# Kernel tuning notes

Measured on AMD Instinct MI355X. Metric: run time of the kernel, lower is better.

## Reference

```python
import jax, jax.numpy as jnp
import numpy as np

B, S, D = 4, 2048, 1024
H = 16
DK = D // H  # 64

def setup_inputs() -> dict:
    key = jax.random.key(0)
    ks = jax.random.split(key, 5)
    scale = 0.02
    return {
        "x": jax.random.normal(ks[0], (B, S, D), dtype=jnp.float32),
        "Wq": jax.random.normal(ks[1], (D, D), dtype=jnp.float32) * scale,
        "Wk": jax.random.normal(ks[2], (D, D), dtype=jnp.float32) * scale,
        "Wv": jax.random.normal(ks[3], (D, D), dtype=jnp.float32) * scale,
        "Wo": jax.random.normal(ks[4], (D, D), dtype=jnp.float32) * scale,
    }

def reference(x, Wq, Wk, Wv, Wo):
    b, s, d = x.shape
    h, dk = H, DK
    # torch nn.Linear(bias=False): y = x @ W.T
    q = (x @ Wq.T).reshape(b, s, h, dk).transpose(0, 2, 1, 3)  # [b,h,s,dk]
    k = (x @ Wk.T).reshape(b, s, h, dk).transpose(0, 2, 1, 3)
    v = (x @ Wv.T).reshape(b, s, h, dk).transpose(0, 2, 1, 3)
    scores = jnp.einsum('bhqd,bhkd->bhqk', q, k) * (dk ** -0.5)
    causal = jnp.triu(jnp.ones((s, s), dtype=bool), k=1)  # True = masked out
    scores = jnp.where(causal, -jnp.inf, scores)
    probs = jax.nn.softmax(scores, axis=-1)
    attn = jnp.einsum('bhqk,bhkd->bhqd', probs, v)  # [b,h,s,dk]
    attn = attn.transpose(0, 2, 1, 3).reshape(b, s, d)
    return attn @ Wo.T
```

## Files before the change

kernel.cpp:

```cpp
#include <hip/hip_runtime.h>

typedef __attribute__((ext_vector_type(8))) short bf16x8;
typedef __attribute__((ext_vector_type(4))) float f32x4;
typedef __attribute__((ext_vector_type(2))) unsigned int u32x2;
typedef unsigned int u32;
typedef unsigned short u16;

constexpr int Bb = 4, S = 2048, D = 1024, H = 16, DK = 64, M = Bb * S;

#if __has_builtin(__builtin_amdgcn_exp2f)
#define EXP2F __builtin_amdgcn_exp2f
#else
#define EXP2F exp2f
#endif

__device__ __forceinline__ u16 f2bf(float f) {
  u32 u = __float_as_uint(f);
  return (u16)((u + 0x7fffu + ((u >> 16) & 1u)) >> 16);
}

__device__ __forceinline__ u32 cvt_pk_bf16(float a, float b) {
  u32 r;
  asm("v_cvt_pk_bf16_f32 %0, %1, %2" : "=v"(r) : "v"(a), "v"(b));
  return r;
}

__device__ __forceinline__ void gld_lds16(const u16* g, u16* l) {
  __builtin_amdgcn_global_load_lds((const __attribute__((address_space(1))) u32*)g,
                                   (__attribute__((address_space(3))) u32*)l, 16, 0, 0);
}

__global__ void cast_kernel(const float* __restrict__ s, u16* __restrict__ d, int n) {
  int i = (blockIdx.x * blockDim.x + threadIdx.x) * 4;
  if (i >= n) return;
  float4 f = *(const float4*)(s + i);
  ushort4 o;
  o.x = f2bf(f.x); o.y = f2bf(f.y); o.z = f2bf(f.z); o.w = f2bf(f.w);
  *(ushort4*)(d + i) = o;
}

struct CastArgs { const float* s[4]; u16* d[4]; float sc[4]; };
__global__ void cast4_kernel(CastArgs a) {
  int i = (blockIdx.x * blockDim.x + threadIdx.x) * 4;
  int w = i >> 20;
  int off = i & ((1 << 20) - 1);
  float sc = a.sc[w];
  float4 f = *(const float4*)(a.s[w] + off);
  ushort4 o;
  o.x = f2bf(f.x * sc); o.y = f2bf(f.y * sc); o.z = f2bf(f.z * sc); o.w = f2bf(f.w * sc);
  *(ushort4*)(a.d[w] + off) = o;
}

template <bool OUTF32>
__device__ __forceinline__ void gemm_core(const u16* __restrict__ A,
                                          const u16* __restrict__ Bt,
                                          float* __restrict__ Cf, u16* __restrict__ Cb,
                                          int Nn, int Kk, int m0, int n0,
                                          u16* As, u16* Bs) {
  const int tid = threadIdx.x, wave = tid >> 6, lane = tid & 63;
  const int quad = lane >> 4, col = lane & 15;
  const int wm = wave >> 1, wn = wave & 1;

  f32x4 acc[4][4];
#pragma unroll
  for (int i = 0; i < 4; i++)
#pragma unroll
    for (int j = 0; j < 4; j++) acc[i][j] = (f32x4){0.f, 0.f, 0.f, 0.f};

  for (int k0 = 0; k0 < Kk; k0 += 64) {
#pragma unroll
    for (int j = 0; j < 4; j++) {
      int g = (wave * 4 + j) * 64;
      int gl = g + lane;
      int r = gl >> 3, sl = gl & 7;
      int kof = (sl ^ (r & 7)) * 8;
      const u16* ga = A + (size_t)(m0 + r) * Kk + k0 + kof;
      gld_lds16(ga, &As[g * 8]);
      const u16* gb = Bt + (size_t)(n0 + r) * Kk + k0 + kof;
      gld_lds16(gb, &Bs[g * 8]);
    }
    __syncthreads();
#pragma unroll
    for (int kb = 0; kb < 2; kb++) {
      bf16x8 af[4], bfr[4];
#pragma unroll
      for (int mi = 0; mi < 4; mi++) {
        int R = wm * 64 + mi * 16 + col;
        af[mi] = *(const bf16x8*)&As[R * 64 + (((kb * 4 + quad) ^ (R & 7)) << 3)];
      }
#pragma unroll
      for (int ni = 0; ni < 4; ni++) {
        int R = wn * 64 + ni * 16 + col;
        bfr[ni] = *(const bf16x8*)&Bs[R * 64 + (((kb * 4 + quad) ^ (R & 7)) << 3)];
      }
#pragma unroll
      for (int mi = 0; mi < 4; mi++)
#pragma unroll
        for (int ni = 0; ni < 4; ni++)
          acc[mi][ni] = __builtin_amdgcn_mfma_f32_16x16x32_bf16(af[mi], bfr[ni], acc[mi][ni], 0, 0, 0);
    }
    __syncthreads();
  }
#pragma unroll
  for (int mi = 0; mi < 4; mi++)
#pragma unroll
    for (int ni = 0; ni < 4; ni++)
#pragma unroll
      for (int r = 0; r < 4; r++) {
        int row = m0 + wm * 64 + mi * 16 + quad * 4 + r;
        int cc = n0 + wn * 64 + ni * 16 + col;
        float v = acc[mi][ni][r];
        if (OUTF32) Cf[(size_t)row * Nn + cc] = v;
        else Cb[(size_t)row * Nn + cc] = f2bf(v);
      }
}

struct QkvArgs { const u16* bt[3]; u16* c[3]; };
__global__ __launch_bounds__(256) void gemm_qkv(const u16* __restrict__ A, QkvArgs q) {
  __shared__ __align__(16) u16 As[128 * 64];
  __shared__ __align__(16) u16 Bs[128 * 64];
  int sel = blockIdx.x >> 3;
  int n0 = (blockIdx.x & 7) * 128, m0 = blockIdx.y * 128;
  gemm_core<false>(A, q.bt[sel], nullptr, q.c[sel], D, D, m0, n0, As, Bs);
}

__global__ __launch_bounds__(256) void gemm_f32(const u16* __restrict__ A,
                                                const u16* __restrict__ Bt,
                                                float* __restrict__ C) {
  __shared__ __align__(16) u16 As[128 * 64];
  __shared__ __align__(16) u16 Bs[128 * 64];
  gemm_core<true>(A, Bt, C, nullptr, D, D, blockIdx.y * 128, blockIdx.x * 128, As, Bs);
}

__global__ __launch_bounds__(256) void attn_kernel(const u16* __restrict__ Q,
                                                   const u16* __restrict__ K,
                                                   const u16* __restrict__ V,
                                                   u16* __restrict__ O) {
  __shared__ __align__(16) u16 Ks[2][2][64 * 32];
  __shared__ __align__(16) u16 Vt[2][64 * 64];
  __shared__ __align__(16) u16 Pw[4][32 * 64];
  const int tid = threadIdx.x, wave = tid >> 6, lane = tid & 63;
  const int quad = lane >> 4, col = lane & 15;
  const int bh = blockIdx.x, b = bh >> 4, h = bh & 15;
  const int pair = blockIdx.y;
  const size_t base = (size_t)b * S * D + h * DK;

  const int vk0 = (tid & 31) * 2;
  const int vdg = tid >> 5;

  bf16x8 bones;
#pragma unroll
  for (int e = 0; e < 8; e++) bones[e] = (short)0x3F80;

  const int rsw = col & 7;
  const int ksl = ((quad ^ ((col >> 1) & 3)) & 3) << 3;
  const u16* kbase[2] = { &Ks[0][0][col * 32 + ksl], &Ks[1][0][col * 32 + ksl] };
  const int vsl0 = ((quad ^ rsw) & 7) << 3;
  const int vsl1 = (((4 + quad) ^ rsw) & 7) << 3;
  const u16* vbase[2] = { &Vt[0][col * 64], &Vt[1][col * 64] };
  u16* pww[2] = { &Pw[wave][col * 64 + (quad & 1) * 4],
                  &Pw[wave][(16 + col) * 64 + (quad & 1) * 4] };
  int swof[4];
#pragma unroll
  for (int n16 = 0; n16 < 4; n16++)
    swof[n16] = (((n16 * 2 + (quad >> 1)) ^ rsw) & 7) << 3;
  const u16* apbase[2] = { &Pw[wave][col * 64], &Pw[wave][(16 + col) * 64] };
  const int kk = tid >> 2;
  const int dch = (tid & 3) ^ ((kk >> 1) & 3);
  const int cb = wave * 64;
  u16* dk[2][2] = { { &Ks[0][0][cb * 8], &Ks[0][1][cb * 8] },
                    { &Ks[1][0][cb * 8], &Ks[1][1][cb * 8] } };
  const int kgrp = vk0 >> 3, kin = vk0 & 7;
  u16* vwb[2] = { &Vt[0][vdg * 8 * 64 + kin], &Vt[1][vdg * 8 * 64 + kin] };
  int vwof[8];
#pragma unroll
  for (int e = 0; e < 8; e++) vwof[e] = e * 64 + ((kgrp ^ e) & 7) * 8;

  auto vstage = [&](const int buf, bf16x8 r0, bf16x8 r1) {
    u16* wb = vwb[buf];
#pragma unroll
    for (int e = 0; e < 8; e++) {
      u32 val = ((u32)(u16)r0[e]) | ((u32)(u16)r1[e] << 16);
      *(u32*)(wb + vwof[e]) = val;
    }
  };

  for (int half = 0; half < 2; half++) {
    const int qb = half ? pair : 15 - pair;
    const int qw = qb * 128 + wave * 32;
    const int nkt = 2 * qb + 2;

    bf16x8 aq[2][2];
#pragma unroll
    for (int mi = 0; mi < 2; mi++)
#pragma unroll
      for (int kb = 0; kb < 2; kb++)
        aq[mi][kb] = *(const bf16x8*)(Q + base + (size_t)(qw + mi * 16 + col) * D + kb * 32 + quad * 8);

    f32x4 ao[2][4], lacc[2];
#pragma unroll
    for (int mi = 0; mi < 2; mi++) {
      lacc[mi] = (f32x4){0.f, 0.f, 0.f, 0.f};
#pragma unroll
      for (int dg = 0; dg < 4; dg++) ao[mi][dg] = (f32x4){0.f, 0.f, 0.f, 0.f};
    }

    auto compute = [&](const int BF, int kt) {
      const u16* kbK = kbase[BF];
      bf16x8 bk0[4], bk1[4];
#pragma unroll
      for (int n16 = 0; n16 < 4; n16++) {
        bk0[n16] = *(const bf16x8*)(kbK + n16 * 512);
        bk1[n16] = *(const bf16x8*)(kbK + n16 * 512 + 2048);
      }
      f32x4 sacc[2][4];
#pragma unroll
      for (int qi = 0; qi < 2; qi++)
#pragma unroll
        for (int n16 = 0; n16 < 4; n16++) sacc[qi][n16] = (f32x4){0.f, 0.f, 0.f, 0.f};
      __builtin_amdgcn_s_setprio(1);
#pragma unroll
      for (int qi = 0; qi < 2; qi++)
#pragma unroll
        for (int n16 = 0; n16 < 4; n16++) {
          sacc[qi][n16] = __builtin_amdgcn_mfma_f32_16x16x32_bf16(bk0[n16], aq[qi][0], sacc[qi][n16], 0, 0, 0);
          sacc[qi][n16] = __builtin_amdgcn_mfma_f32_16x16x32_bf16(bk1[n16], aq[qi][1], sacc[qi][n16], 0, 0, 0);
        }
      __builtin_amdgcn_s_setprio(0);
      const bool full = (kt * 64 + 63) <= qw;
#pragma unroll
      for (int qi = 0; qi < 2; qi++) {
        const int qg = qw + qi * 16 + col;
#pragma unroll
        for (int n16 = 0; n16 < 4; n16++) {
          float p0 = EXP2F(sacc[qi][n16][0]);
          float p1 = EXP2F(sacc[qi][n16][1]);
          float p2 = EXP2F(sacc[qi][n16][2]);
          float p3 = EXP2F(sacc[qi][n16][3]);
          if (!full) {
            int kg = kt * 64 + n16 * 16 + quad * 4;
            p0 = (kg + 0 > qg) ? 0.f : p0;
            p1 = (kg + 1 > qg) ? 0.f : p1;
            p2 = (kg + 2 > qg) ? 0.f : p2;
            p3 = (kg + 3 > qg) ? 0.f : p3;
          }
          u32 lo = cvt_pk_bf16(p0, p1);
          u32 hi = cvt_pk_bf16(p2, p3);
          *(u32x2*)(pww[qi] + swof[n16]) = (u32x2){lo, hi};
        }
      }
      const u16* vtB = vbase[BF];
      bf16x8 bv0[4], bv1[4];
#pragma unroll
      for (int dg = 0; dg < 4; dg++) {
        bv0[dg] = *(const bf16x8*)(vtB + dg * 1024 + vsl0);
        bv1[dg] = *(const bf16x8*)(vtB + dg * 1024 + vsl1);
      }
#pragma unroll
      for (int mi = 0; mi < 2; mi++) {
        bf16x8 ap0 = *(const bf16x8*)(apbase[mi] + vsl0);
        bf16x8 ap1 = *(const bf16x8*)(apbase[mi] + vsl1);
        __builtin_amdgcn_s_setprio(1);
#pragma unroll
        for (int dg = 0; dg < 4; dg++) {
          ao[mi][dg] = __builtin_amdgcn_mfma_f32_16x16x32_bf16(ap0, bv0[dg], ao[mi][dg], 0, 0, 0);
          ao[mi][dg] = __builtin_amdgcn_mfma_f32_16x16x32_bf16(ap1, bv1[dg], ao[mi][dg], 0, 0, 0);
        }
        lacc[mi] = __builtin_amdgcn_mfma_f32_16x16x32_bf16(ap0, bones, lacc[mi], 0, 0, 0);
        lacc[mi] = __builtin_amdgcn_mfma_f32_16x16x32_bf16(ap1, bones, lacc[mi], 0, 0, 0);
        __builtin_amdgcn_s_setprio(0);
      }
    };

    bf16x8 vA0, vA1, vB0, vB1;
    const u16* gv = V + base + (size_t)vk0 * D + vdg * 8;
    vA0 = *(const bf16x8*)gv;
    vA1 = *(const bf16x8*)(gv + D);
    __syncthreads();
    const u16* gk = K + base + (size_t)kk * D + dch * 8;
    gld_lds16(gk, dk[0][0]);
    gld_lds16(gk + 32, dk[0][1]);
    gk += (size_t)64 * D;
    vstage(0, vA0, vA1);
    vB0 = *(const bf16x8*)(gv + (size_t)64 * D);
    vB1 = *(const bf16x8*)(gv + (size_t)64 * D + D);
    gv += (size_t)128 * D;

    for (int kt = 0; kt < nkt; kt += 2) {
      __syncthreads();
      {
        gld_lds16(gk, dk[1][0]);
        gld_lds16(gk + 32, dk[1][1]);
        gk += (size_t)64 * D;
        vstage(1, vB0, vB1);
        if (kt + 2 < nkt) {
          vA0 = *(const bf16x8*)gv;
          vA1 = *(const bf16x8*)(gv + D);
          gv += (size_t)64 * D;
        }
        if (kt * 64 <= qw + 31) compute(0, kt);
      }
      __syncthreads();
      {
        const int kt1 = kt + 1;
        if (kt1 + 1 < nkt) {
          gld_lds16(gk, dk[0][0]);
          gld_lds16(gk + 32, dk[0][1]);
          gk += (size_t)64 * D;
          vstage(0, vA0, vA1);
          if (kt1 + 2 < nkt) {
            vB0 = *(const bf16x8*)gv;
            vB1 = *(const bf16x8*)(gv + D);
            gv += (size_t)64 * D;
          }
        }
        if (kt1 * 64 <= qw + 31) compute(1, kt1);
      }
    }
#pragma unroll
    for (int mi = 0; mi < 2; mi++)
#pragma unroll
      for (int r = 0; r < 4; r++) {
        float inv = 1.f / lacc[mi][r];
        int q = qw + mi * 16 + quad * 4 + r;
#pragma unroll
        for (int dg = 0; dg < 4; dg++)
          O[base + (size_t)q * D + dg * 16 + col] = f2bf(ao[mi][dg][r] * inv);
      }
  }
}

extern "C" void kernel_launch(void* const* d_in, const int* in_sizes, int n_in,
                              void* d_out, int out_size, void* d_ws, size_t ws_size,
                              hipStream_t stream) {
  const float* x  = (const float*)d_in[0];
  const float* Wq = (const float*)d_in[1];
  const float* Wk = (const float*)d_in[2];
  const float* Wv = (const float*)d_in[3];
  const float* Wo = (const float*)d_in[4];

  u16* xb  = (u16*)d_ws;
  u16* wqb = xb + (size_t)M * D;
  u16* wkb = wqb + (size_t)D * D;
  u16* wvb = wkb + (size_t)D * D;
  u16* wob = wvb + (size_t)D * D;
  u16* Qb  = wob + (size_t)D * D;
  u16* Kb  = Qb + (size_t)M * D;
  u16* Vb  = Kb + (size_t)M * D;
  u16* Ab  = xb;

  cast_kernel<<<M * D / 1024, 256, 0, stream>>>(x, xb, M * D);
  CastArgs ca;
  ca.s[0] = Wq; ca.s[1] = Wk; ca.s[2] = Wv; ca.s[3] = Wo;
  ca.d[0] = wqb; ca.d[1] = wkb; ca.d[2] = wvb; ca.d[3] = wob;
  ca.sc[0] = 0.18033688011112042f;
  ca.sc[1] = 1.f; ca.sc[2] = 1.f; ca.sc[3] = 1.f;
  cast4_kernel<<<4 * D * D / 1024, 256, 0, stream>>>(ca);

  QkvArgs qa;
  qa.bt[0] = wqb; qa.bt[1] = wkb; qa.bt[2] = wvb;
  qa.c[0] = Qb; qa.c[1] = Kb; qa.c[2] = Vb;
  gemm_qkv<<<dim3(24, M / 128), 256, 0, stream>>>(xb, qa);

  attn_kernel<<<dim3(Bb * H, 8), 256, 0, stream>>>(Qb, Kb, Vb, Ab);

  gemm_f32<<<dim3(D / 128, M / 128), 256, 0, stream>>>(Ab, wob, (float*)d_out);
}
```

Baseline: 247.4 us.

## Stage 128-key blocks per barrier in attention and merge cast kernels

```diff
diff --git a/kernel.cpp b/kernel.cpp
--- a/kernel.cpp
+++ b/kernel.cpp
@@ -30,20 +30,12 @@
                                    (__attribute__((address_space(3))) u32*)l, 16, 0, 0);
 }
 
-__global__ void cast_kernel(const float* __restrict__ s, u16* __restrict__ d, int n) {
-  int i = (blockIdx.x * blockDim.x + threadIdx.x) * 4;
-  if (i >= n) return;
-  float4 f = *(const float4*)(s + i);
-  ushort4 o;
-  o.x = f2bf(f.x); o.y = f2bf(f.y); o.z = f2bf(f.z); o.w = f2bf(f.w);
-  *(ushort4*)(d + i) = o;
-}
-
-struct CastArgs { const float* s[4]; u16* d[4]; float sc[4]; };
-__global__ void cast4_kernel(CastArgs a) {
-  int i = (blockIdx.x * blockDim.x + threadIdx.x) * 4;
-  int w = i >> 20;
-  int off = i & ((1 << 20) - 1);
+struct CastAll { const float* s[5]; u16* d[5]; float sc[5]; };
+__global__ __launch_bounds__(256) void cast_all_kernel(CastAll a) {
+  int bid = blockIdx.x;
+  int w, off;
+  if (bid < 4096) { w = bid >> 10; off = ((bid & 1023) * 256 + threadIdx.x) * 4; }
+  else            { w = 4;         off = ((bid - 4096) * 256 + threadIdx.x) * 4; }
   float sc = a.sc[w];
   float4 f = *(const float4*)(a.s[w] + off);
   ushort4 o;
@@ -136,8 +128,8 @@
                                                    const u16* __restrict__ K,
                                                    const u16* __restrict__ V,
                                                    u16* __restrict__ O) {
-  __shared__ __align__(16) u16 Ks[2][2][64 * 32];
-  __shared__ __align__(16) u16 Vt[2][64 * 64];
+  __shared__ __align__(16) u16 Ks[2][2][2][64 * 32];
+  __shared__ __align__(16) u16 Vt[2][2][64 * 64];
   __shared__ __align__(16) u16 Pw[4][32 * 64];
   const int tid = threadIdx.x, wave = tid >> 6, lane = tid & 63;
   const int quad = lane >> 4, col = lane & 15;
@@ -154,10 +146,22 @@
 
   const int rsw = col & 7;
   const int ksl = ((quad ^ ((col >> 1) & 3)) & 3) << 3;
-  const u16* kbase[2] = { &Ks[0][0][col * 32 + ksl], &Ks[1][0][col * 32 + ksl] };
+  const u16* kbase[2][2];
+  const u16* vbase[2][2];
+  u16* dk[2][2][2];
+  u16* vwb[2][2];
+#pragma unroll
+  for (int bu = 0; bu < 2; bu++)
+#pragma unroll
+    for (int kh = 0; kh < 2; kh++) {
+      kbase[bu][kh] = &Ks[bu][kh][0][col * 32 + ksl];
+      vbase[bu][kh] = &Vt[bu][kh][col * 64];
+      dk[bu][kh][0] = &Ks[bu][kh][0][wave * 64 * 8];
+      dk[bu][kh][1] = &Ks[bu][kh][1][wave * 64 * 8];
+      vwb[bu][kh] = &Vt[bu][kh][vdg * 8 * 64 + (vk0 & 7)];
+    }
   const int vsl0 = ((quad ^ rsw) & 7) << 3;
   const int vsl1 = (((4 + quad) ^ rsw) & 7) << 3;
-  const u16* vbase[2] = { &Vt[0][col * 64], &Vt[1][col * 64] };
   u16* pww[2] = { &Pw[wave][col * 64 + (quad & 1) * 4],
                   &Pw[wave][(16 + col) * 64 + (quad & 1) * 4] };
   int swof[4];
@@ -167,17 +171,12 @@
   const u16* apbase[2] = { &Pw[wave][col * 64], &Pw[wave][(16 + col) * 64] };
   const int kk = tid >> 2;
   const int dch = (tid & 3) ^ ((kk >> 1) & 3);
-  const int cb = wave * 64;
-  u16* dk[2][2] = { { &Ks[0][0][cb * 8], &Ks[0][1][cb * 8] },
-                    { &Ks[1][0][cb * 8], &Ks[1][1][cb * 8] } };
-  const int kgrp = vk0 >> 3, kin = vk0 & 7;
-  u16* vwb[2] = { &Vt[0][vdg * 8 * 64 + kin], &Vt[1][vdg * 8 * 64 + kin] };
+  const int kgrp = vk0 >> 3;
   int vwof[8];
 #pragma unroll
   for (int e = 0; e < 8; e++) vwof[e] = e * 64 + ((kgrp ^ e) & 7) * 8;
 
-  auto vstage = [&](const int buf, bf16x8 r0, bf16x8 r1) {
-    u16* wb = vwb[buf];
+  auto vstage = [&](u16* wb, bf16x8 r0, bf16x8 r1) {
 #pragma unroll
     for (int e = 0; e < 8; e++) {
       u32 val = ((u32)(u16)r0[e]) | ((u32)(u16)r1[e] << 16);
@@ -188,7 +187,7 @@
   for (int half = 0; half < 2; half++) {
     const int qb = half ? pair : 15 - pair;
     const int qw = qb * 128 + wave * 32;
-    const int nkt = 2 * qb + 2;
+    const int n128 = qb + 1;
 
     bf16x8 aq[2][2];
 #pragma unroll
@@ -205,8 +204,8 @@
       for (int dg = 0; dg < 4; dg++) ao[mi][dg] = (f32x4){0.f, 0.f, 0.f, 0.f};
     }
 
-    auto compute = [&](const int BF, int kt) {
-      const u16* kbK = kbase[BF];
+    auto compute = [&](const int BF, const int HH, int kt) {
+      const u16* kbK = kbase[BF][HH];
       bf16x8 bk0[4], bk1[4];
 #pragma unroll
       for (int n16 = 0; n16 < 4; n16++) {
@@ -249,7 +248,7 @@
           *(u32x2*)(pww[qi] + swof[n16]) = (u32x2){lo, hi};
         }
       }
-      const u16* vtB = vbase[BF];
+      const u16* vtB = vbase[BF][HH];
       bf16x8 bv0[4], bv1[4];
 #pragma unroll
       for (int dg = 0; dg < 4; dg++) {
@@ -272,50 +271,69 @@
       }
     };
 
-    bf16x8 vA0, vA1, vB0, vB1;
+    bf16x8 vA0, vA1, vA2, vA3, vB0, vB1, vB2, vB3;
     const u16* gv = V + base + (size_t)vk0 * D + vdg * 8;
     vA0 = *(const bf16x8*)gv;
     vA1 = *(const bf16x8*)(gv + D);
+    vA2 = *(const bf16x8*)(gv + (size_t)64 * D);
+    vA3 = *(const bf16x8*)(gv + (size_t)65 * D);
     __syncthreads();
     const u16* gk = K + base + (size_t)kk * D + dch * 8;
-    gld_lds16(gk, dk[0][0]);
-    gld_lds16(gk + 32, dk[0][1]);
-    gk += (size_t)64 * D;
-    vstage(0, vA0, vA1);
-    vB0 = *(const bf16x8*)(gv + (size_t)64 * D);
-    vB1 = *(const bf16x8*)(gv + (size_t)64 * D + D);
-    gv += (size_t)128 * D;
-
-    for (int kt = 0; kt < nkt; kt += 2) {
+    gld_lds16(gk, dk[0][0][0]);
+    gld_lds16(gk + 32, dk[0][0][1]);
+    gld_lds16(gk + (size_t)64 * D, dk[0][1][0]);
+    gld_lds16(gk + (size_t)64 * D + 32, dk[0][1][1]);
+    gk += (size_t)128 * D;
+    vstage(vwb[0][0], vA0, vA1);
+    vstage(vwb[0][1], vA2, vA3);
+    if (n128 > 1) {
+      vB0 = *(const bf16x8*)(gv + (size_t)128 * D);
+      vB1 = *(const bf16x8*)(gv + (size_t)129 * D);
+      vB2 = *(const bf16x8*)(gv + (size_t)192 * D);
+      vB3 = *(const bf16x8*)(gv + (size_t)193 * D);
+    }
+    gv += (size_t)256 * D;
+
+    for (int t2 = 0; t2 < n128; t2 += 2) {
       __syncthreads();
-      {
-        gld_lds16(gk, dk[1][0]);
-        gld_lds16(gk + 32, dk[1][1]);
-        gk += (size_t)64 * D;
-        vstage(1, vB0, vB1);
-        if (kt + 2 < nkt) {
+      if (t2 + 1 < n128) {
+        gld_lds16(gk, dk[1][0][0]);
+        gld_lds16(gk + 32, dk[1][0][1]);
+        gld_lds16(gk + (size_t)64 * D, dk[1][1][0]);
+        gld_lds16(gk + (size_t)64 * D + 32, dk[1][1][1]);
+        gk += (size_t)128 * D;
+        vstage(vwb[1][0], vB0, vB1);
+        vstage(vwb[1][1], vB2, vB3);
+        if (t2 + 2 < n128) {
           vA0 = *(const bf16x8*)gv;
           vA1 = *(const bf16x8*)(gv + D);
-          gv += (size_t)64 * D;
-        }
-        if (kt * 64 <= qw + 31) compute(0, kt);
-      }
+          vA2 = *(const bf16x8*)(gv + (size_t)64 * D);
+          vA3 = *(const bf16x8*)(gv + (size_t)65 * D);
+          gv += (size_t)128 * D;
+        }
+      }
+      compute(0, 0, 2 * t2);
+      if ((2 * t2 + 1) * 64 <= qw + 31) compute(0, 1, 2 * t2 + 1);
+      if (t2 + 1 >= n128) break;
       __syncthreads();
-      {
-        const int kt1 = kt + 1;
-        if (kt1 + 1 < nkt) {
-          gld_lds16(gk, dk[0][0]);
-          gld_lds16(gk + 32, dk[0][1]);
-          gk += (size_t)64 * D;
-          vstage(0, vA0, vA1);
-          if (kt1 + 2 < nkt) {
-            vB0 = *(const bf16x8*)gv;
-            vB1 = *(const bf16x8*)(gv + D);
-            gv += (size_t)64 * D;
-          }
-        }
-        if (kt1 * 64 <= qw + 31) compute(1, kt1);
-      }
+      if (t2 + 2 < n128) {
+        gld_lds16(gk, dk[0][0][0]);
+        gld_lds16(gk + 32, dk[0][0][1]);
+        gld_lds16(gk + (size_t)64 * D, dk[0][1][0]);
+        gld_lds16(gk + (size_t)64 * D + 32, dk[0][1][1]);
+        gk += (size_t)128 * D;
+        vstage(vwb[0][0], vA0, vA1);
+        vstage(vwb[0][1], vA2, vA3);
+        if (t2 + 3 < n128) {
+          vB0 = *(const bf16x8*)gv;
+          vB1 = *(const bf16x8*)(gv + D);
+          vB2 = *(const bf16x8*)(gv + (size_t)64 * D);
+          vB3 = *(const bf16x8*)(gv + (size_t)65 * D);
+          gv += (size_t)128 * D;
+        }
+      }
+      compute(1, 0, 2 * (t2 + 1));
+      if ((2 * (t2 + 1) + 1) * 64 <= qw + 31) compute(1, 1, 2 * (t2 + 1) + 1);
     }
 #pragma unroll
     for (int mi = 0; mi < 2; mi++)
@@ -349,13 +367,12 @@
   u16* Vb  = Kb + (size_t)M * D;
   u16* Ab  = xb;
 
-  cast_kernel<<<M * D / 1024, 256, 0, stream>>>(x, xb, M * D);
-  CastArgs ca;
-  ca.s[0] = Wq; ca.s[1] = Wk; ca.s[2] = Wv; ca.s[3] = Wo;
-  ca.d[0] = wqb; ca.d[1] = wkb; ca.d[2] = wvb; ca.d[3] = wob;
+  CastAll ca;
+  ca.s[0] = Wq; ca.s[1] = Wk; ca.s[2] = Wv; ca.s[3] = Wo; ca.s[4] = x;
+  ca.d[0] = wqb; ca.d[1] = wkb; ca.d[2] = wvb; ca.d[3] = wob; ca.d[4] = xb;
   ca.sc[0] = 0.18033688011112042f;
-  ca.sc[1] = 1.f; ca.sc[2] = 1.f; ca.sc[3] = 1.f;
-  cast4_kernel<<<4 * D * D / 1024, 256, 0, stream>>>(ca);
+  ca.sc[1] = 1.f; ca.sc[2] = 1.f; ca.sc[3] = 1.f; ca.sc[4] = 1.f;
+  cast_all_kernel<<<4096 + M * D / 1024, 256, 0, stream>>>(ca);
 
   QkvArgs qa;
   qa.bt[0] = wqb; qa.bt[1] = wkb; qa.bt[2] = wvb;
```

Result: slower. 261.5 us (+5.7%).

## Keep attention probabilities in registers via 16x16x16 MFMA; merge cast kernels

Applied to the files above, without the earlier changes.

```diff
diff --git a/kernel.cpp b/kernel.cpp
--- a/kernel.cpp
+++ b/kernel.cpp
@@ -1,8 +1,8 @@
 #include <hip/hip_runtime.h>
 
 typedef __attribute__((ext_vector_type(8))) short bf16x8;
+typedef __attribute__((ext_vector_type(4))) short bf16x4;
 typedef __attribute__((ext_vector_type(4))) float f32x4;
-typedef __attribute__((ext_vector_type(2))) unsigned int u32x2;
 typedef unsigned int u32;
 typedef unsigned short u16;
 
@@ -25,25 +25,26 @@
   return r;
 }
 
+__device__ __forceinline__ f32x4 mfma16(bf16x4 a, bf16x4 b, f32x4 c) {
+#if __has_builtin(__builtin_amdgcn_mfma_f32_16x16x16bf16_1k)
+  return __builtin_amdgcn_mfma_f32_16x16x16bf16_1k(a, b, c, 0, 0, 0);
+#else
+  asm("v_mfma_f32_16x16x16_bf16 %0, %1, %2, %0" : "+v"(c) : "v"(a), "v"(b));
+  return c;
+#endif
+}
+
 __device__ __forceinline__ void gld_lds16(const u16* g, u16* l) {
   __builtin_amdgcn_global_load_lds((const __attribute__((address_space(1))) u32*)g,
                                    (__attribute__((address_space(3))) u32*)l, 16, 0, 0);
 }
 
-__global__ void cast_kernel(const float* __restrict__ s, u16* __restrict__ d, int n) {
-  int i = (blockIdx.x * blockDim.x + threadIdx.x) * 4;
-  if (i >= n) return;
-  float4 f = *(const float4*)(s + i);
-  ushort4 o;
-  o.x = f2bf(f.x); o.y = f2bf(f.y); o.z = f2bf(f.z); o.w = f2bf(f.w);
-  *(ushort4*)(d + i) = o;
-}
-
-struct CastArgs { const float* s[4]; u16* d[4]; float sc[4]; };
-__global__ void cast4_kernel(CastArgs a) {
-  int i = (blockIdx.x * blockDim.x + threadIdx.x) * 4;
-  int w = i >> 20;
-  int off = i & ((1 << 20) - 1);
+struct CastAll { const float* s[5]; u16* d[5]; float sc[5]; };
+__global__ __launch_bounds__(256) void cast_all_kernel(CastAll a) {
+  int bid = blockIdx.x;
+  int w, off;
+  if (bid < 4096) { w = bid >> 10; off = ((bid & 1023) * 256 + threadIdx.x) * 4; }
+  else            { w = 4;         off = ((bid - 4096) * 256 + threadIdx.x) * 4; }
   float sc = a.sc[w];
   float4 f = *(const float4*)(a.s[w] + off);
   ushort4 o;
@@ -138,7 +139,6 @@
                                                    u16* __restrict__ O) {
   __shared__ __align__(16) u16 Ks[2][2][64 * 32];
   __shared__ __align__(16) u16 Vt[2][64 * 64];
-  __shared__ __align__(16) u16 Pw[4][32 * 64];
   const int tid = threadIdx.x, wave = tid >> 6, lane = tid & 63;
   const int quad = lane >> 4, col = lane & 15;
   const int bh = blockIdx.x, b = bh >> 4, h = bh & 15;
@@ -148,23 +148,19 @@
   const int vk0 = (tid & 31) * 2;
   const int vdg = tid >> 5;
 
-  bf16x8 bones;
-#pragma unroll
-  for (int e = 0; e < 8; e++) bones[e] = (short)0x3F80;
+  bf16x4 bones4;
+#pragma unroll
+  for (int e = 0; e < 4; e++) bones4[e] = (short)0x3F80;
 
   const int rsw = col & 7;
   const int ksl = ((quad ^ ((col >> 1) & 3)) & 3) << 3;
   const u16* kbase[2] = { &Ks[0][0][col * 32 + ksl], &Ks[1][0][col * 32 + ksl] };
-  const int vsl0 = ((quad ^ rsw) & 7) << 3;
-  const int vsl1 = (((4 + quad) ^ rsw) & 7) << 3;
-  const u16* vbase[2] = { &Vt[0][col * 64], &Vt[1][col * 64] };
-  u16* pww[2] = { &Pw[wave][col * 64 + (quad & 1) * 4],
-                  &Pw[wave][(16 + col) * 64 + (quad & 1) * 4] };
-  int swof[4];
+  const u16* vbase16[2] = { &Vt[0][col * 64 + ((quad & 1) << 2)],
+                            &Vt[1][col * 64 + ((quad & 1) << 2)] };
+  int slof[4];
 #pragma unroll
   for (int n16 = 0; n16 < 4; n16++)
-    swof[n16] = (((n16 * 2 + (quad >> 1)) ^ rsw) & 7) << 3;
-  const u16* apbase[2] = { &Pw[wave][col * 64], &Pw[wave][(16 + col) * 64] };
+    slof[n16] = (((2 * n16 + (quad >> 1)) ^ rsw) & 7) << 3;
   const int kk = tid >> 2;
   const int dch = (tid & 3) ^ ((kk >> 1) & 3);
   const int cb = wave * 64;
@@ -228,6 +224,7 @@
         }
       __builtin_amdgcn_s_setprio(0);
       const bool full = (kt * 64 + 63) <= qw;
+      bf16x4 ap[2][4];
 #pragma unroll
       for (int qi = 0; qi < 2; qi++) {
         const int qg = qw + qi * 16 + col;
@@ -244,30 +241,27 @@
             p2 = (kg + 2 > qg) ? 0.f : p2;
             p3 = (kg + 3 > qg) ? 0.f : p3;
           }
-          u32 lo = cvt_pk_bf16(p0, p1);
-          u32 hi = cvt_pk_bf16(p2, p3);
-          *(u32x2*)(pww[qi] + swof[n16]) = (u32x2){lo, hi};
-        }
-      }
-      const u16* vtB = vbase[BF];
-      bf16x8 bv0[4], bv1[4];
-#pragma unroll
-      for (int dg = 0; dg < 4; dg++) {
-        bv0[dg] = *(const bf16x8*)(vtB + dg * 1024 + vsl0);
-        bv1[dg] = *(const bf16x8*)(vtB + dg * 1024 + vsl1);
-      }
-#pragma unroll
-      for (int mi = 0; mi < 2; mi++) {
-        bf16x8 ap0 = *(const bf16x8*)(apbase[mi] + vsl0);
-        bf16x8 ap1 = *(const bf16x8*)(apbase[mi] + vsl1);
+          union { u32 u[2]; bf16x4 v; } pk;
+          pk.u[0] = cvt_pk_bf16(p0, p1);
+          pk.u[1] = cvt_pk_bf16(p2, p3);
+          ap[qi][n16] = pk.v;
+        }
+      }
+      const u16* vtB = vbase16[BF];
+#pragma unroll
+      for (int n16 = 0; n16 < 4; n16++) {
+        bf16x4 bv[4];
+#pragma unroll
+        for (int dg = 0; dg < 4; dg++)
+          bv[dg] = *(const bf16x4*)(vtB + dg * 1024 + slof[n16]);
         __builtin_amdgcn_s_setprio(1);
 #pragma unroll
-        for (int dg = 0; dg < 4; dg++) {
-          ao[mi][dg] = __builtin_amdgcn_mfma_f32_16x16x32_bf16(ap0, bv0[dg], ao[mi][dg], 0, 0, 0);
-          ao[mi][dg] = __builtin_amdgcn_mfma_f32_16x16x32_bf16(ap1, bv1[dg], ao[mi][dg], 0, 0, 0);
-        }
-        lacc[mi] = __builtin_amdgcn_mfma_f32_16x16x32_bf16(ap0, bones, lacc[mi], 0, 0, 0);
-        lacc[mi] = __builtin_amdgcn_mfma_f32_16x16x32_bf16(ap1, bones, lacc[mi], 0, 0, 0);
+        for (int mi = 0; mi < 2; mi++) {
+#pragma unroll
+          for (int dg = 0; dg < 4; dg++)
+            ao[mi][dg] = mfma16(ap[mi][n16], bv[dg], ao[mi][dg]);
+          lacc[mi] = mfma16(ap[mi][n16], bones4, lacc[mi]);
+        }
         __builtin_amdgcn_s_setprio(0);
       }
     };
@@ -349,13 +343,12 @@
   u16* Vb  = Kb + (size_t)M * D;
   u16* Ab  = xb;
 
-  cast_kernel<<<M * D / 1024, 256, 0, stream>>>(x, xb, M * D);
-  CastArgs ca;
-  ca.s[0] = Wq; ca.s[1] = Wk; ca.s[2] = Wv; ca.s[3] = Wo;
-  ca.d[0] = wqb; ca.d[1] = wkb; ca.d[2] = wvb; ca.d[3] = wob;
+  CastAll ca;
+  ca.s[0] = Wq; ca.s[1] = Wk; ca.s[2] = Wv; ca.s[3] = Wo; ca.s[4] = x;
+  ca.d[0] = wqb; ca.d[1] = wkb; ca.d[2] = wvb; ca.d[3] = wob; ca.d[4] = xb;
   ca.sc[0] = 0.18033688011112042f;
-  ca.sc[1] = 1.f; ca.sc[2] = 1.f; ca.sc[3] = 1.f;
-  cast4_kernel<<<4 * D * D / 1024, 256, 0, stream>>>(ca);
+  ca.sc[1] = 1.f; ca.sc[2] = 1.f; ca.sc[3] = 1.f; ca.sc[4] = 1.f;
+  cast_all_kernel<<<4096 + M * D / 1024, 256, 0, stream>>>(ca);
 
   QkvArgs qa;
   qa.bt[0] = wqb; qa.bt[1] = wkb; qa.bt[2] = wvb;
```

Result: no change. 251.3 us (+1.6%).

## Double-buffer GEMM LDS tiles with 256x128 blocks and merge cast kernels

Applied to the files above, without the earlier changes.

```diff
diff --git a/kernel.cpp b/kernel.cpp
--- a/kernel.cpp
+++ b/kernel.cpp
@@ -30,20 +30,12 @@
                                    (__attribute__((address_space(3))) u32*)l, 16, 0, 0);
 }
 
-__global__ void cast_kernel(const float* __restrict__ s, u16* __restrict__ d, int n) {
-  int i = (blockIdx.x * blockDim.x + threadIdx.x) * 4;
-  if (i >= n) return;
-  float4 f = *(const float4*)(s + i);
-  ushort4 o;
-  o.x = f2bf(f.x); o.y = f2bf(f.y); o.z = f2bf(f.z); o.w = f2bf(f.w);
-  *(ushort4*)(d + i) = o;
-}
-
-struct CastArgs { const float* s[4]; u16* d[4]; float sc[4]; };
-__global__ void cast4_kernel(CastArgs a) {
-  int i = (blockIdx.x * blockDim.x + threadIdx.x) * 4;
-  int w = i >> 20;
-  int off = i & ((1 << 20) - 1);
+struct CastAll { const float* s[5]; u16* d[5]; float sc[5]; };
+__global__ __launch_bounds__(256) void cast_all_kernel(CastAll a) {
+  int bid = blockIdx.x;
+  int w, off;
+  if (bid < 4096) { w = bid >> 10; off = ((bid & 1023) * 256 + threadIdx.x) * 4; }
+  else            { w = 4;         off = ((bid - 4096) * 256 + threadIdx.x) * 4; }
   float sc = a.sc[w];
   float4 f = *(const float4*)(a.s[w] + off);
   ushort4 o;
@@ -52,55 +44,128 @@
 }
 
 template <bool OUTF32>
-__device__ __forceinline__ void gemm_core(const u16* __restrict__ A,
+__device__ __forceinline__ void gemm_body(const u16* __restrict__ A,
                                           const u16* __restrict__ Bt,
                                           float* __restrict__ Cf, u16* __restrict__ Cb,
-                                          int Nn, int Kk, int m0, int n0,
-                                          u16* As, u16* Bs) {
+                                          int m0, int n0, u16* As0, u16* As1,
+                                          u16* Bs0, u16* Bs1) {
+  constexpr int K = 1024;
   const int tid = threadIdx.x, wave = tid >> 6, lane = tid & 63;
   const int quad = lane >> 4, col = lane & 15;
   const int wm = wave >> 1, wn = wave & 1;
 
+  const u16* pA[4];
+  u16* dA0[4]; u16* dA1[4];
+#pragma unroll
+  for (int j = 0; j < 4; j++) {
+    int gl = tid + j * 512;
+    int r = gl >> 3, sl = gl & 7;
+    int kof = (sl ^ (r & 7)) * 8;
+    pA[j] = A + (size_t)(m0 + r) * K + kof;
+    dA0[j] = As0 + gl * 8; dA1[j] = As1 + gl * 8;
+  }
+  const u16* pB[2];
+  u16* dB0[2]; u16* dB1[2];
+#pragma unroll
+  for (int j = 0; j < 2; j++) {
+    int gl = tid + j * 512;
+    int r = gl >> 3, sl = gl & 7;
+    int kof = (sl ^ (r & 7)) * 8;
+    pB[j] = Bt + (size_t)(n0 + r) * K + kof;
+    dB0[j] = Bs0 + gl * 8; dB1[j] = Bs1 + gl * 8;
+  }
+  const u16* rdA0[4]; const u16* rdA1[4];
+  const u16* rdB0[4]; const u16* rdB1[4];
+#pragma unroll
+  for (int mi = 0; mi < 4; mi++) {
+    int R = wm * 64 + mi * 16 + col;
+    rdA0[mi] = As0 + R * 64 + ((quad ^ (R & 7)) << 3);
+    rdA1[mi] = As1 + R * 64 + ((quad ^ (R & 7)) << 3);
+  }
+#pragma unroll
+  for (int ni = 0; ni < 4; ni++) {
+    int R = wn * 64 + ni * 16 + col;
+    rdB0[ni] = Bs0 + R * 64 + ((quad ^ (R & 7)) << 3);
+    rdB1[ni] = Bs1 + R * 64 + ((quad ^ (R & 7)) << 3);
+  }
+  int dkbA[4], dkbB[4];
+#pragma unroll
+  for (int mi = 0; mi < 4; mi++) {
+    int R = wm * 64 + mi * 16 + col;
+    dkbA[mi] = ((((4 + quad) ^ (R & 7)) - (quad ^ (R & 7))) << 3);
+  }
+#pragma unroll
+  for (int ni = 0; ni < 4; ni++) {
+    int R = wn * 64 + ni * 16 + col;
+    dkbB[ni] = ((((4 + quad) ^ (R & 7)) - (quad ^ (R & 7))) << 3);
+  }
+
   f32x4 acc[4][4];
 #pragma unroll
   for (int i = 0; i < 4; i++)
 #pragma unroll
     for (int j = 0; j < 4; j++) acc[i][j] = (f32x4){0.f, 0.f, 0.f, 0.f};
 
-  for (int k0 = 0; k0 < Kk; k0 += 64) {
-#pragma unroll
-    for (int j = 0; j < 4; j++) {
-      int g = (wave * 4 + j) * 64;
-      int gl = g + lane;
-      int r = gl >> 3, sl = gl & 7;
-      int kof = (sl ^ (r & 7)) * 8;
-      const u16* ga = A + (size_t)(m0 + r) * Kk + k0 + kof;
-      gld_lds16(ga, &As[g * 8]);
-      const u16* gb = Bt + (size_t)(n0 + r) * Kk + k0 + kof;
-      gld_lds16(gb, &Bs[g * 8]);
-    }
-    __syncthreads();
-#pragma unroll
-    for (int kb = 0; kb < 2; kb++) {
-      bf16x8 af[4], bfr[4];
-#pragma unroll
-      for (int mi = 0; mi < 4; mi++) {
-        int R = wm * 64 + mi * 16 + col;
-        af[mi] = *(const bf16x8*)&As[R * 64 + (((kb * 4 + quad) ^ (R & 7)) << 3)];
-      }
-#pragma unroll
-      for (int ni = 0; ni < 4; ni++) {
-        int R = wn * 64 + ni * 16 + col;
-        bfr[ni] = *(const bf16x8*)&Bs[R * 64 + (((kb * 4 + quad) ^ (R & 7)) << 3)];
-      }
+  auto stage = [&](u16* const* dA, u16* const* dB) {
+#pragma unroll
+    for (int j = 0; j < 4; j++) gld_lds16(pA[j], dA[j]);
+#pragma unroll
+    for (int j = 0; j < 2; j++) gld_lds16(pB[j], dB[j]);
+#pragma unroll
+    for (int j = 0; j < 4; j++) pA[j] += 64;
+#pragma unroll
+    for (int j = 0; j < 2; j++) pB[j] += 64;
+  };
+
+  auto compute = [&](const u16* const* rdA, const u16* const* rdB) {
+    bf16x8 af[4][2], bfr[4][2];
+#pragma unroll
+    for (int mi = 0; mi < 4; mi++) {
+      af[mi][0] = *(const bf16x8*)(rdA[mi]);
+      af[mi][1] = *(const bf16x8*)(rdA[mi] + dkbA[mi]);
+    }
+#pragma unroll
+    for (int ni = 0; ni < 4; ni++) {
+      bfr[ni][0] = *(const bf16x8*)(rdB[ni]);
+      bfr[ni][1] = *(const bf16x8*)(rdB[ni] + dkbB[ni]);
+    }
+#pragma unroll
+    for (int kb = 0; kb < 2; kb++)
 #pragma unroll
       for (int mi = 0; mi < 4; mi++)
 #pragma unroll
         for (int ni = 0; ni < 4; ni++)
-          acc[mi][ni] = __builtin_amdgcn_mfma_f32_16x16x32_bf16(af[mi], bfr[ni], acc[mi][ni], 0, 0, 0);
-    }
-    __syncthreads();
-  }
+          acc[mi][ni] = __builtin_amdgcn_mfma_f32_16x16x32_bf16(af[mi][kb], bfr[ni][kb], acc[mi][ni], 0, 0, 0);
+  };
+
+  stage(dA0, dB0);
+
+#pragma unroll 1
+  for (int t2 = 0; t2 < 8; t2++) {
+    __builtin_amdgcn_sched_barrier(0);
+    __builtin_amdgcn_s_barrier();
+    __builtin_amdgcn_sched_barrier(0);
+    stage(dA1, dB1);
+    asm volatile("s_waitcnt vmcnt(6)" ::: "memory");
+    __builtin_amdgcn_sched_barrier(0);
+    __builtin_amdgcn_s_barrier();
+    __builtin_amdgcn_sched_barrier(0);
+    compute(rdA0, rdB0);
+    __builtin_amdgcn_sched_barrier(0);
+    __builtin_amdgcn_s_barrier();
+    __builtin_amdgcn_sched_barrier(0);
+    if (t2 < 7) {
+      stage(dA0, dB0);
+      asm volatile("s_waitcnt vmcnt(6)" ::: "memory");
+    } else {
+      asm volatile("s_waitcnt vmcnt(0)" ::: "memory");
+    }
+    __builtin_amdgcn_sched_barrier(0);
+    __builtin_amdgcn_s_barrier();
+    __builtin_amdgcn_sched_barrier(0);
+    compute(rdA1, rdB1);
+  }
+
 #pragma unroll
   for (int mi = 0; mi < 4; mi++)
 #pragma unroll
@@ -110,26 +175,26 @@
         int row = m0 + wm * 64 + mi * 16 + quad * 4 + r;
         int cc = n0 + wn * 64 + ni * 16 + col;
         float v = acc[mi][ni][r];
-        if (OUTF32) Cf[(size_t)row * Nn + cc] = v;
-        else Cb[(size_t)row * Nn + cc] = f2bf(v);
+        if (OUTF32) Cf[(size_t)row * D + cc] = v;
+        else Cb[(size_t)row * D + cc] = f2bf(v);
       }
 }
 
 struct QkvArgs { const u16* bt[3]; u16* c[3]; };
-__global__ __launch_bounds__(256) void gemm_qkv(const u16* __restrict__ A, QkvArgs q) {
-  __shared__ __align__(16) u16 As[128 * 64];
-  __shared__ __align__(16) u16 Bs[128 * 64];
+__global__ __launch_bounds__(512) void gemm_qkv(const u16* __restrict__ A, QkvArgs q) {
+  __shared__ __align__(16) u16 As[2][256 * 64];
+  __shared__ __align__(16) u16 Bs[2][128 * 64];
   int sel = blockIdx.x >> 3;
-  int n0 = (blockIdx.x & 7) * 128, m0 = blockIdx.y * 128;
-  gemm_core<false>(A, q.bt[sel], nullptr, q.c[sel], D, D, m0, n0, As, Bs);
-}
-
-__global__ __launch_bounds__(256) void gemm_f32(const u16* __restrict__ A,
+  int n0 = (blockIdx.x & 7) * 128, m0 = blockIdx.y * 256;
+  gemm_body<false>(A, q.bt[sel], nullptr, q.c[sel], m0, n0, As[0], As[1], Bs[0], Bs[1]);
+}
+
+__global__ __launch_bounds__(512) void gemm_f32(const u16* __restrict__ A,
                                                 const u16* __restrict__ Bt,
                                                 float* __restrict__ C) {
-  __shared__ __align__(16) u16 As[128 * 64];
-  __shared__ __align__(16) u16 Bs[128 * 64];
-  gemm_core<true>(A, Bt, C, nullptr, D, D, blockIdx.y * 128, blockIdx.x * 128, As, Bs);
+  __shared__ __align__(16) u16 As[2][256 * 64];
+  __shared__ __align__(16) u16 Bs[2][128 * 64];
+  gemm_body<true>(A, Bt, C, nullptr, blockIdx.y * 256, blockIdx.x * 128, As[0], As[1], Bs[0], Bs[1]);
 }
 
 __global__ __launch_bounds__(256) void attn_kernel(const u16* __restrict__ Q,
@@ -349,20 +414,19 @@
   u16* Vb  = Kb + (size_t)M * D;
   u16* Ab  = xb;
 
-  cast_kernel<<<M * D / 1024, 256, 0, stream>>>(x, xb, M * D);
-  CastArgs ca;
-  ca.s[0] = Wq; ca.s[1] = Wk; ca.s[2] = Wv; ca.s[3] = Wo;
-  ca.d[0] = wqb; ca.d[1] = wkb; ca.d[2] = wvb; ca.d[3] = wob;
+  CastAll ca;
+  ca.s[0] = Wq; ca.s[1] = Wk; ca.s[2] = Wv; ca.s[3] = Wo; ca.s[4] = x;
+  ca.d[0] = wqb; ca.d[1] = wkb; ca.d[2] = wvb; ca.d[3] = wob; ca.d[4] = xb;
   ca.sc[0] = 0.18033688011112042f;
-  ca.sc[1] = 1.f; ca.sc[2] = 1.f; ca.sc[3] = 1.f;
-  cast4_kernel<<<4 * D * D / 1024, 256, 0, stream>>>(ca);
+  ca.sc[1] = 1.f; ca.sc[2] = 1.f; ca.sc[3] = 1.f; ca.sc[4] = 1.f;
+  cast_all_kernel<<<4096 + M * D / 1024, 256, 0, stream>>>(ca);
 
   QkvArgs qa;
   qa.bt[0] = wqb; qa.bt[1] = wkb; qa.bt[2] = wvb;
   qa.c[0] = Qb; qa.c[1] = Kb; qa.c[2] = Vb;
-  gemm_qkv<<<dim3(24, M / 128), 256, 0, stream>>>(xb, qa);
+  gemm_qkv<<<dim3(24, M / 256), 512, 0, stream>>>(xb, qa);
 
   attn_kernel<<<dim3(Bb * H, 8), 256, 0, stream>>>(Qb, Kb, Vb, Ab);
 
-  gemm_f32<<<dim3(D / 128, M / 128), 256, 0, stream>>>(Ab, wob, (float*)d_out);
-}
+  gemm_f32<<<dim3(D / 128, M / 256), 512, 0, stream>>>(Ab, wob, (float*)d_out);
+}
```

New measurement: 248.6 us. Within noise of the previous version (+0.5%).
